# Kernel tuning notes

Hardware: AMD Instinct MI355X
Metric: run time of the kernel (lower is better)

## Reference

```python
import jax, jax.numpy as jnp
import numpy as np

# Config constants from source
L_LAYERS = 4      # n_layer
C = 228           # n_embed
LANES = 4         # SSM.lanes
HD = C // LANES   # head_dim = 57
V = 50257         # vocab_size
B, T = 2, 1024


def _ln(x, g, eps=1e-5):
    # LayerNorm with no bias (bias=False in Block/modules.LayerNorm)
    m = jnp.mean(x, axis=-1, keepdims=True)
    var = jnp.mean((x - m) ** 2, axis=-1, keepdims=True)
    return (x - m) * jax.lax.rsqrt(var + eps) * g


def _rms(z, eps=1e-6):
    # utils.rms: RMS-normalize along last dim
    return z * jax.lax.rsqrt(jnp.mean(z * z, axis=-1, keepdims=True) + eps)


def _combine(left, right, w_orth):
    # SSM.get_scan combine op: per-position lane attention + orthogonal mix + residual
    Bc, Tc, Cc = left.shape
    q = left.reshape(Bc, Tc, LANES, HD)
    k = right.reshape(Bc, Tc, LANES, HD)
    # scanner(left, right, weight): orthogonal butterfly mix of the pair
    v = jnp.einsum('btc,cd->btd', left + right, w_orth).reshape(Bc, Tc, LANES, HD)
    # SDPA over the lane axis (seq length = LANES, feature = HD)
    scores = jnp.einsum('btld,btmd->btlm', q, k) / jnp.sqrt(jnp.float32(HD))
    att = jax.nn.softmax(scores, axis=-1)
    z = jnp.einsum('btlm,btmd->btld', att, v)
    denom = (1.0 + jnp.arange(LANES, dtype=z.dtype)).reshape(1, 1, LANES, 1)
    z = _rms(z) / denom
    return left + z.reshape(Bc, Tc, Cc)


def _pscan2(x, w_orth, ident):
    # log-depth (Kogge-Stone) inclusive scan along time with identity fill
    ident_b = jnp.broadcast_to(ident, x.shape)
    Tn = x.shape[1]
    off = 1
    while off < Tn:  # static python loop: ceil(log2(T)) combine steps
        left = jnp.concatenate([ident_b[:, :off], x[:, :-off]], axis=1)
        x = _combine(left, x, w_orth)
        off *= 2
    return x


def _forward(idx, wte, ln1_g, ln2_g, w_up, w_v, w_cproj, w_scan, ident, w_fc, w_proj):
    x = wte[idx]  # [B,T,C]
    for i in range(L_LAYERS):
        h = _ln(x, ln1_g[i])
        qin = h @ w_up[i].T          # SSM.up
        v = h @ w_v[i].T             # SSM.v_attn
        q = _pscan2(qin, w_scan[i], ident[i])
        y = (q * v) @ w_cproj[i].T   # SSM.c_proj (dropout = identity in eval)
        x = x + y
        h2 = _ln(x, ln2_g[i])
        x = x + jax.nn.gelu(h2 @ w_fc[i].T) @ w_proj[i].T  # MLP
    # lm_head tied to wte (non-Train path applies lm_head directly)
    return x @ wte.T


def setup_inputs() -> dict:
    key = jax.random.key(0)
    ks = jax.random.split(key, 10)
    s = 0.02
    wte = jax.random.normal(ks[0], (V, C), dtype=jnp.float32) * s
    ln1_g = jnp.ones((L_LAYERS, C), dtype=jnp.float32)
    ln2_g = jnp.ones((L_LAYERS, C), dtype=jnp.float32)
    w_up = jax.random.normal(ks[1], (L_LAYERS, C, C), dtype=jnp.float32) * s
    w_v = jax.random.normal(ks[2], (L_LAYERS, C, C), dtype=jnp.float32) * s
    w_cproj = jax.random.normal(ks[3], (L_LAYERS, C, C), dtype=jnp.float32) * s
    # orthogonal scanner weights (compute_orthogonal_weights) via QR
    a = jax.random.normal(ks[4], (L_LAYERS, C, C), dtype=jnp.float32)
    w_scan, _ = jnp.linalg.qr(a)
    ident = jax.random.uniform(ks[5], (L_LAYERS, C), dtype=jnp.float32)  # nn.Parameter(torch.rand)
    w_fc = jax.random.normal(ks[6], (L_LAYERS, 4 * C, C), dtype=jnp.float32) * s
    w_proj = jax.random.normal(ks[7], (L_LAYERS, C, 4 * C), dtype=jnp.float32) * s
    idx = jax.random.randint(ks[8], (B, T), 0, V, dtype=jnp.int64)
    return {"idx": idx, "wte": wte, "ln1_g": ln1_g, "ln2_g": ln2_g, "w_up": w_up,
            "w_v": w_v, "w_cproj": w_cproj, "w_scan": w_scan, "ident": ident,
            "w_fc": w_fc, "w_proj": w_proj}


def reference(idx, wte, ln1_g, ln2_g, w_up, w_v, w_cproj, w_scan, ident, w_fc, w_proj):
    return _forward(idx, wte, ln1_g, ln2_g, w_up, w_v, w_cproj, w_scan, ident, w_fc, w_proj)
```

## Files before the change

### kernel.cpp

```cpp
#include <hip/hip_runtime.h>
#include <hip/hip_bf16.h>

#define C       228
#define TT      1024
#define NPOS    2048
#define LANESN  4
#define HD      57
#define VOC     50257
#define KPAD    256
#define HID     912
#define NLAYER  4

typedef __bf16 bf16x8 __attribute__((ext_vector_type(8)));
typedef float  f32x4  __attribute__((ext_vector_type(4)));

__device__ __forceinline__ float rdl(float v, int lane) {
    return __int_as_float(__builtin_amdgcn_readlane(__float_as_int(v), lane));
}

__global__ void transpose_k(const float* __restrict__ src, float* __restrict__ dst,
                            int R, int Cc, int dstStride, int dstColOff,
                            int srcLayerStride, int dstLayerStride) {
    int layer = blockIdx.y;
    src += (size_t)layer * srcLayerStride;
    dst += (size_t)layer * dstLayerStride;
    int i = blockIdx.x * 256 + threadIdx.x;
    if (i < R * Cc) {
        int r = i / Cc, c = i - r * Cc;
        dst[(size_t)c * dstStride + dstColOff + r] = src[i];
    }
}

__global__ void embed_k(const int* __restrict__ idx, const float* __restrict__ wte,
                        float* __restrict__ x) {
    int i = blockIdx.x * 256 + threadIdx.x;
    int n = i / C, c = i - n * C;
    x[i] = wte[(size_t)idx[n] * C + c];
}

__global__ __launch_bounds__(512) void lnuv_k(const float* __restrict__ x, const float* __restrict__ g,
                                              const float* __restrict__ wuvT,
                                              float* __restrict__ qout, float* __restrict__ vout) {
    __shared__ __align__(16) float hsh[8][256];
    int tid = threadIdx.x, nb = blockIdx.x * 8;
    int wv = tid >> 6, ln = tid & 63;
    const float* xr = x + (size_t)(nb + wv) * C;
    float vals[4]; float s = 0.f, ss = 0.f;
#pragma unroll
    for (int j = 0; j < 4; ++j) {
        int c = ln + 64 * j;
        float vv = (c < C) ? xr[c] : 0.f;
        vals[j] = vv; s += vv; ss += vv * vv;
    }
#pragma unroll
    for (int o = 32; o > 0; o >>= 1) { s += __shfl_xor(s, o, 64); ss += __shfl_xor(ss, o, 64); }
    float mean = s * (1.f / C);
    float rstd = rsqrtf(ss * (1.f / C) - mean * mean + 1e-5f);
#pragma unroll
    for (int j = 0; j < 4; ++j) {
        int c = ln + 64 * j;
        hsh[wv][c] = (c < C) ? (vals[j] - mean) * rstd * g[c] : 0.f;
    }
    __syncthreads();
    f32x4 hv[8];
#pragma unroll
    for (int p = 0; p < 8; ++p) hv[p] = *(const f32x4*)&hsh[p][4 * ln];
    int col  = tid;
    int colc = (col < 2 * C) ? col : 0;
    float acc[8] = {0,0,0,0,0,0,0,0};
    const float* wcol = wuvT + colc;
    for (int c4 = 0; c4 < 57; ++c4) {
        float w0 = wcol[(size_t)(c4 * 4 + 0) * (2 * C)];
        float w1 = wcol[(size_t)(c4 * 4 + 1) * (2 * C)];
        float w2 = wcol[(size_t)(c4 * 4 + 2) * (2 * C)];
        float w3 = wcol[(size_t)(c4 * 4 + 3) * (2 * C)];
#pragma unroll
        for (int p = 0; p < 8; ++p) {
            acc[p] = fmaf(rdl(hv[p].x, c4), w0, acc[p]);
            acc[p] = fmaf(rdl(hv[p].y, c4), w1, acc[p]);
            acc[p] = fmaf(rdl(hv[p].z, c4), w2, acc[p]);
            acc[p] = fmaf(rdl(hv[p].w, c4), w3, acc[p]);
        }
    }
    if (col < C) {
#pragma unroll
        for (int p = 0; p < 8; ++p) qout[(size_t)(nb + p) * C + col] = acc[p];
    } else if (col < 2 * C) {
#pragma unroll
        for (int p = 0; p < 8; ++p) vout[(size_t)(nb + p) * C + col - C] = acc[p];
    }
}

__global__ __launch_bounds__(512) void scan_k(const float* __restrict__ src, float* __restrict__ dst,
                                              const float* __restrict__ wscan,
                                              const float* __restrict__ ident, int off) {
    __shared__ __align__(16) float lsh[8][232];
    __shared__ __align__(16) float rsh[8][232];
    __shared__ __align__(16) float ush[8][256];
    __shared__ __align__(16) float vmsh[8][232];
    __shared__ __align__(16) float zsh[8][232];
    int tid = threadIdx.x;
    int nb  = blockIdx.x * 8;
    int wv = tid >> 6, ln = tid & 63;
    for (int i = tid; i < 8 * C; i += 512) {
        int p = i / C, c = i - p * C;
        int n = nb + p, t = n & (TT - 1);
        float r = src[(size_t)nb * C + i];
        float l = (t >= off) ? src[(size_t)(n - off) * C + c] : ident[c];
        lsh[p][c] = l; rsh[p][c] = r; ush[p][c] = l + r;
    }
    if (tid < 256) { int p = tid >> 5, c = 228 + (tid & 31); if (c < 256) ush[p][c] = 0.f; }
    __syncthreads();
    {
        int half = (tid >= 256) ? 4 : 0;
        int col  = tid & 255;
        int colc = (col < C) ? col : 0;
        f32x4 hv0 = *(const f32x4*)&ush[half + 0][4 * ln];
        f32x4 hv1 = *(const f32x4*)&ush[half + 1][4 * ln];
        f32x4 hv2 = *(const f32x4*)&ush[half + 2][4 * ln];
        f32x4 hv3 = *(const f32x4*)&ush[half + 3][4 * ln];
        float a0 = 0.f, a1 = 0.f, a2 = 0.f, a3 = 0.f;
        const float* wcol = wscan + colc;
        for (int c4 = 0; c4 < 57; ++c4) {
            float w0 = wcol[(size_t)(c4 * 4 + 0) * C];
            float w1 = wcol[(size_t)(c4 * 4 + 1) * C];
            float w2 = wcol[(size_t)(c4 * 4 + 2) * C];
            float w3 = wcol[(size_t)(c4 * 4 + 3) * C];
            a0 = fmaf(rdl(hv0.x, c4), w0, a0); a0 = fmaf(rdl(hv0.y, c4), w1, a0);
            a0 = fmaf(rdl(hv0.z, c4), w2, a0); a0 = fmaf(rdl(hv0.w, c4), w3, a0);
            a1 = fmaf(rdl(hv1.x, c4), w0, a1); a1 = fmaf(rdl(hv1.y, c4), w1, a1);
            a1 = fmaf(rdl(hv1.z, c4), w2, a1); a1 = fmaf(rdl(hv1.w, c4), w3, a1);
            a2 = fmaf(rdl(hv2.x, c4), w0, a2); a2 = fmaf(rdl(hv2.y, c4), w1, a2);
            a2 = fmaf(rdl(hv2.z, c4), w2, a2); a2 = fmaf(rdl(hv2.w, c4), w3, a2);
            a3 = fmaf(rdl(hv3.x, c4), w0, a3); a3 = fmaf(rdl(hv3.y, c4), w1, a3);
            a3 = fmaf(rdl(hv3.z, c4), w2, a3); a3 = fmaf(rdl(hv3.w, c4), w3, a3);
        }
        if (col < C) {
            vmsh[half + 0][col] = a0; vmsh[half + 1][col] = a1;
            vmsh[half + 2][col] = a2; vmsh[half + 3][col] = a3;
        }
    }
    __syncthreads();
    float att = 0.f;
    {
        int l = (ln >> 2) & 3, m = ln & 3;
        float sc = 0.f;
        if (ln < 16) {
            const float* qv = &lsh[wv][l * HD];
            const float* kv = &rsh[wv][m * HD];
            for (int d = 0; d < HD; ++d) sc = fmaf(qv[d], kv[d], sc);
            sc *= 0.13245323570650439f;
        }
        float mx = fmaxf(sc, __shfl_xor(sc, 1, 4));
        mx = fmaxf(mx, __shfl_xor(mx, 2, 4));
        float e = expf(sc - mx);
        float se = e + __shfl_xor(e, 1, 4);
        se += __shfl_xor(se, 2, 4);
        att = e / se;
    }
    float zreg[4];
    int lidx[4];
#pragma unroll
    for (int j = 0; j < 4; ++j) {
        int c = ln + 64 * j;
        zreg[j] = 0.f; lidx[j] = 0;
        if (c < C) {
            int l = (c >= 171) + (c >= 114) + (c >= 57);
            int d = c - 57 * l;
            float b0 = __shfl(att, 4 * l + 0, 64);
            float b1 = __shfl(att, 4 * l + 1, 64);
            float b2 = __shfl(att, 4 * l + 2, 64);
            float b3 = __shfl(att, 4 * l + 3, 64);
            float z = b0 * vmsh[wv][d] + b1 * vmsh[wv][HD + d]
                    + b2 * vmsh[wv][2 * HD + d] + b3 * vmsh[wv][3 * HD + d];
            zsh[wv][c] = z; zreg[j] = z; lidx[j] = l;
        }
    }
    float rs = 0.f;
    if (ln < 4) {
        float zz = 0.f;
        const float* zr = &zsh[wv][ln * HD];
        for (int d = 0; d < HD; ++d) zz = fmaf(zr[d], zr[d], zz);
        rs = rsqrtf(zz * (1.f / HD) + 1e-6f) / (float)(1 + ln);
    }
#pragma unroll
    for (int j = 0; j < 4; ++j) {
        int c = ln + 64 * j;
        if (c < C) {
            float rsl = __shfl(rs, lidx[j], 64);
            dst[(size_t)(nb + wv) * C + c] = lsh[wv][c] + zreg[j] * rsl;
        }
    }
}

__global__ __launch_bounds__(512) void cproj_k(const float* __restrict__ q, const float* __restrict__ v,
                                               const float* __restrict__ wcT, float* __restrict__ x) {
    __shared__ __align__(16) float psh[8][256];
    int tid = threadIdx.x, nb = blockIdx.x * 8;
    int ln = tid & 63;
    for (int i = tid; i < 8 * 256; i += 512) {
        int p = i >> 8, c = i & 255;
        psh[p][c] = (c < C) ? q[(size_t)(nb + p) * C + c] * v[(size_t)(nb + p) * C + c] : 0.f;
    }
    __syncthreads();
    int half = (tid >= 256) ? 4 : 0;
    int col  = tid & 255;
    int colc = (col < C) ? col : 0;
    f32x4 hv0 = *(const f32x4*)&psh[half + 0][4 * ln];
    f32x4 hv1 = *(const f32x4*)&psh[half + 1][4 * ln];
    f32x4 hv2 = *(const f32x4*)&psh[half + 2][4 * ln];
    f32x4 hv3 = *(const f32x4*)&psh[half + 3][4 * ln];
    float a0 = 0.f, a1 = 0.f, a2 = 0.f, a3 = 0.f;
    const float* wcol = wcT + colc;
    for (int c4 = 0; c4 < 57; ++c4) {
        float w0 = wcol[(size_t)(c4 * 4 + 0) * C];
        float w1 = wcol[(size_t)(c4 * 4 + 1) * C];
        float w2 = wcol[(size_t)(c4 * 4 + 2) * C];
        float w3 = wcol[(size_t)(c4 * 4 + 3) * C];
        a0 = fmaf(rdl(hv0.x, c4), w0, a0); a0 = fmaf(rdl(hv0.y, c4), w1, a0);
        a0 = fmaf(rdl(hv0.z, c4), w2, a0); a0 = fmaf(rdl(hv0.w, c4), w3, a0);
        a1 = fmaf(rdl(hv1.x, c4), w0, a1); a1 = fmaf(rdl(hv1.y, c4), w1, a1);
        a1 = fmaf(rdl(hv1.z, c4), w2, a1); a1 = fmaf(rdl(hv1.w, c4), w3, a1);
        a2 = fmaf(rdl(hv2.x, c4), w0, a2); a2 = fmaf(rdl(hv2.y, c4), w1, a2);
        a2 = fmaf(rdl(hv2.z, c4), w2, a2); a2 = fmaf(rdl(hv2.w, c4), w3, a2);
        a3 = fmaf(rdl(hv3.x, c4), w0, a3); a3 = fmaf(rdl(hv3.y, c4), w1, a3);
        a3 = fmaf(rdl(hv3.z, c4), w2, a3); a3 = fmaf(rdl(hv3.w, c4), w3, a3);
    }
    if (col < C) {
        x[(size_t)(nb + half + 0) * C + col] += a0;
        x[(size_t)(nb + half + 1) * C + col] += a1;
        x[(size_t)(nb + half + 2) * C + col] += a2;
        x[(size_t)(nb + half + 3) * C + col] += a3;
    }
}

__global__ __launch_bounds__(512) void lnfc_k(const float* __restrict__ x, const float* __restrict__ g,
                                              const float* __restrict__ wfcT, float* __restrict__ hid) {
    __shared__ __align__(16) float hsh[8][256];
    int tid = threadIdx.x, nb = blockIdx.x * 8;
    int wv = tid >> 6, ln = tid & 63;
    const float* xr = x + (size_t)(nb + wv) * C;
    float vals[4]; float s = 0.f, ss = 0.f;
#pragma unroll
    for (int j = 0; j < 4; ++j) {
        int c = ln + 64 * j;
        float vv = (c < C) ? xr[c] : 0.f;
        vals[j] = vv; s += vv; ss += vv * vv;
    }
#pragma unroll
    for (int o = 32; o > 0; o >>= 1) { s += __shfl_xor(s, o, 64); ss += __shfl_xor(ss, o, 64); }
    float mean = s * (1.f / C);
    float rstd = rsqrtf(ss * (1.f / C) - mean * mean + 1e-5f);
#pragma unroll
    for (int j = 0; j < 4; ++j) {
        int c = ln + 64 * j;
        hsh[wv][c] = (c < C) ? (vals[j] - mean) * rstd * g[c] : 0.f;
    }
    __syncthreads();
    f32x4 hv[8];
#pragma unroll
    for (int p = 0; p < 8; ++p) hv[p] = *(const f32x4*)&hsh[p][4 * ln];
    int c0 = tid;
    int c1 = tid + 512;
    int c1c = (c1 < HID) ? c1 : 0;
    float acc0[8] = {0,0,0,0,0,0,0,0};
    float acc1[8] = {0,0,0,0,0,0,0,0};
    const float* w0p = wfcT + c0;
    const float* w1p = wfcT + c1c;
    for (int c4 = 0; c4 < 57; ++c4) {
        float wa0 = w0p[(size_t)(c4 * 4 + 0) * HID];
        float wa1 = w0p[(size_t)(c4 * 4 + 1) * HID];
        float wa2 = w0p[(size_t)(c4 * 4 + 2) * HID];
        float wa3 = w0p[(size_t)(c4 * 4 + 3) * HID];
        float wb0 = w1p[(size_t)(c4 * 4 + 0) * HID];
        float wb1 = w1p[(size_t)(c4 * 4 + 1) * HID];
        float wb2 = w1p[(size_t)(c4 * 4 + 2) * HID];
        float wb3 = w1p[(size_t)(c4 * 4 + 3) * HID];
#pragma unroll
        for (int p = 0; p < 8; ++p) {
            float h0 = rdl(hv[p].x, c4), h1 = rdl(hv[p].y, c4);
            float h2 = rdl(hv[p].z, c4), h3 = rdl(hv[p].w, c4);
            acc0[p] = fmaf(h0, wa0, acc0[p]); acc0[p] = fmaf(h1, wa1, acc0[p]);
            acc0[p] = fmaf(h2, wa2, acc0[p]); acc0[p] = fmaf(h3, wa3, acc0[p]);
            acc1[p] = fmaf(h0, wb0, acc1[p]); acc1[p] = fmaf(h1, wb1, acc1[p]);
            acc1[p] = fmaf(h2, wb2, acc1[p]); acc1[p] = fmaf(h3, wb3, acc1[p]);
        }
    }
#pragma unroll
    for (int p = 0; p < 8; ++p) {
        float u = acc0[p];
        float th = tanhf(0.7978845608028654f * (u + 0.044715f * u * u * u));
        hid[(size_t)(nb + p) * HID + c0] = 0.5f * u * (1.f + th);
    }
    if (c1 < HID) {
#pragma unroll
        for (int p = 0; p < 8; ++p) {
            float u = acc1[p];
            float th = tanhf(0.7978845608028654f * (u + 0.044715f * u * u * u));
            hid[(size_t)(nb + p) * HID + c1] = 0.5f * u * (1.f + th);
        }
    }
}

__global__ __launch_bounds__(512) void proj_k(const float* __restrict__ hid,
                                              const float* __restrict__ wpT, float* __restrict__ x) {
    __shared__ __align__(16) float hsh[8][944];
    int tid = threadIdx.x, nb = blockIdx.x * 8;
    int ln = tid & 63;
    for (int i = tid; i < 8 * HID; i += 512) {
        int p = i / HID, c = i - p * HID;
        hsh[p][c] = hid[(size_t)nb * HID + i];
    }
    if (tid < 256) { int p = tid >> 5; hsh[p][912 + (tid & 31)] = 0.f; }
    __syncthreads();
    int half = (tid >= 256) ? 4 : 0;
    int col  = tid & 255;
    int colc = (col < C) ? col : 0;
    float a0 = 0.f, a1 = 0.f, a2 = 0.f, a3 = 0.f;
    const float* wcol = wpT + colc;
    for (int ch = 0; ch < 4; ++ch) {
        f32x4 hv0 = *(const f32x4*)&hsh[half + 0][228 * ch + 4 * ln];
        f32x4 hv1 = *(const f32x4*)&hsh[half + 1][228 * ch + 4 * ln];
        f32x4 hv2 = *(const f32x4*)&hsh[half + 2][228 * ch + 4 * ln];
        f32x4 hv3 = *(const f32x4*)&hsh[half + 3][228 * ch + 4 * ln];
        const float* wch = wcol + (size_t)(228 * ch) * C;
        for (int c4 = 0; c4 < 57; ++c4) {
            float w0 = wch[(size_t)(c4 * 4 + 0) * C];
            float w1 = wch[(size_t)(c4 * 4 + 1) * C];
            float w2 = wch[(size_t)(c4 * 4 + 2) * C];
            float w3 = wch[(size_t)(c4 * 4 + 3) * C];
            a0 = fmaf(rdl(hv0.x, c4), w0, a0); a0 = fmaf(rdl(hv0.y, c4), w1, a0);
            a0 = fmaf(rdl(hv0.z, c4), w2, a0); a0 = fmaf(rdl(hv0.w, c4), w3, a0);
            a1 = fmaf(rdl(hv1.x, c4), w0, a1); a1 = fmaf(rdl(hv1.y, c4), w1, a1);
            a1 = fmaf(rdl(hv1.z, c4), w2, a1); a1 = fmaf(rdl(hv1.w, c4), w3, a1);
            a2 = fmaf(rdl(hv2.x, c4), w0, a2); a2 = fmaf(rdl(hv2.y, c4), w1, a2);
            a2 = fmaf(rdl(hv2.z, c4), w2, a2); a2 = fmaf(rdl(hv2.w, c4), w3, a2);
            a3 = fmaf(rdl(hv3.x, c4), w0, a3); a3 = fmaf(rdl(hv3.y, c4), w1, a3);
            a3 = fmaf(rdl(hv3.z, c4), w2, a3); a3 = fmaf(rdl(hv3.w, c4), w3, a3);
        }
    }
    if (col < C) {
        x[(size_t)(nb + half + 0) * C + col] += a0;
        x[(size_t)(nb + half + 1) * C + col] += a1;
        x[(size_t)(nb + half + 2) * C + col] += a2;
        x[(size_t)(nb + half + 3) * C + col] += a3;
    }
}

__global__ void convx_k(const float* __restrict__ x, __hip_bfloat16* __restrict__ xbf) {
    int i = blockIdx.x * 256 + threadIdx.x;
    int n = i >> 8, c = i & 255;
    xbf[i] = __float2bfloat16((c < C) ? x[(size_t)n * C + c] : 0.f);
}
__global__ void convw_k(const float* __restrict__ wte, __hip_bfloat16* __restrict__ wbf) {
    size_t i = (size_t)blockIdx.x * 256 + threadIdx.x;
    size_t n = i >> 8; int c = (int)(i & 255);
    wbf[i] = __float2bfloat16((c < C) ? wte[n * C + c] : 0.f);
}

__global__ __launch_bounds__(256) void lmhead_k(const __bf16* __restrict__ A,
                                                const __bf16* __restrict__ Bw,
                                                float* __restrict__ out) {
    int lane = threadIdx.x & 63;
    int wave = threadIdx.x >> 6;
    int wm = wave >> 1, wn = wave & 1;
    int m0 = blockIdx.x * 128 + wm * 64;
    int n0 = blockIdx.y * 128 + wn * 64;
    int r  = lane & 15, q = lane >> 4;
    f32x4 acc[4][4] = {};
    const __bf16* Ap = A + (size_t)(m0 + r) * KPAD + q * 8;
    int brow[4];
#pragma unroll
    for (int nt = 0; nt < 4; ++nt) { int rw = n0 + nt * 16 + r; brow[nt] = (rw < VOC) ? rw : 0; }
    for (int kc = 0; kc < 8; ++kc) {
        int ko = kc * 32;
        bf16x8 a[4], b[4];
#pragma unroll
        for (int mt = 0; mt < 4; ++mt)
            a[mt] = *(const bf16x8*)(Ap + (size_t)mt * 16 * KPAD + ko);
#pragma unroll
        for (int nt = 0; nt < 4; ++nt)
            b[nt] = *(const bf16x8*)(Bw + (size_t)brow[nt] * KPAD + q * 8 + ko);
#pragma unroll
        for (int mt = 0; mt < 4; ++mt)
#pragma unroll
            for (int nt = 0; nt < 4; ++nt)
                acc[mt][nt] = __builtin_amdgcn_mfma_f32_16x16x32_bf16(a[mt], b[nt], acc[mt][nt], 0, 0, 0);
    }
#pragma unroll
    for (int mt = 0; mt < 4; ++mt)
#pragma unroll
        for (int nt = 0; nt < 4; ++nt) {
            int col = n0 + nt * 16 + r;
            if (col < VOC) {
#pragma unroll
                for (int rr = 0; rr < 4; ++rr) {
                    int row = m0 + mt * 16 + q * 4 + rr;
                    out[(size_t)row * VOC + col] = acc[mt][nt][rr];
                }
            }
        }
}

extern "C" void kernel_launch(void* const* d_in, const int* in_sizes, int n_in,
                              void* d_out, int out_size, void* d_ws, size_t ws_size,
                              hipStream_t stream) {
    const int*   idx     = (const int*)d_in[0];
    const float* wte     = (const float*)d_in[1];
    const float* ln1_g   = (const float*)d_in[2];
    const float* ln2_g   = (const float*)d_in[3];
    const float* w_up    = (const float*)d_in[4];
    const float* w_v     = (const float*)d_in[5];
    const float* w_cproj = (const float*)d_in[6];
    const float* w_scan  = (const float*)d_in[7];
    const float* identp  = (const float*)d_in[8];
    const float* w_fc    = (const float*)d_in[9];
    const float* w_proj  = (const float*)d_in[10];
    float* out = (float*)d_out;

    float* ws   = (float*)d_ws;
    float* x    = ws;
    float* buf0 = x    + (size_t)NPOS * C;
    float* buf1 = buf0 + (size_t)NPOS * C;
    float* vbuf = buf1 + (size_t)NPOS * C;
    float* hid  = vbuf + (size_t)NPOS * C;
    float* wuvT = hid  + (size_t)NPOS * HID;
    float* wcT  = wuvT + (size_t)NLAYER * C * 2 * C;
    float* wfcT = wcT  + (size_t)NLAYER * C * C;
    float* wpT  = wfcT + (size_t)NLAYER * C * HID;
    __hip_bfloat16* xbf   = (__hip_bfloat16*)(wpT + (size_t)NLAYER * HID * C);
    __hip_bfloat16* wtebf = xbf + (size_t)NPOS * KPAD;

    dim3 tg1((C * C + 255) / 256, NLAYER);
    transpose_k<<<tg1, 256, 0, stream>>>(w_up,    wuvT, C, C, 2 * C, 0, C * C, C * 2 * C);
    transpose_k<<<tg1, 256, 0, stream>>>(w_v,     wuvT, C, C, 2 * C, C, C * C, C * 2 * C);
    transpose_k<<<tg1, 256, 0, stream>>>(w_cproj, wcT,  C, C, C,     0, C * C, C * C);
    dim3 tg2((HID * C + 255) / 256, NLAYER);
    transpose_k<<<tg2, 256, 0, stream>>>(w_fc,   wfcT, HID, C, HID, 0, HID * C, C * HID);
    transpose_k<<<tg2, 256, 0, stream>>>(w_proj, wpT,  C, HID, C,   0, C * HID, HID * C);

    embed_k<<<NPOS * C / 256, 256, 0, stream>>>(idx, wte, x);

    for (int L = 0; L < NLAYER; ++L) {
        lnuv_k<<<NPOS / 8, 512, 0, stream>>>(x, ln1_g + L * C, wuvT + (size_t)L * C * 2 * C, buf0, vbuf);
        float* cur = buf0; float* oth = buf1;
        for (int off = 1; off < TT; off <<= 1) {
            scan_k<<<NPOS / 8, 512, 0, stream>>>(cur, oth, w_scan + (size_t)L * C * C, identp + L * C, off);
            float* tmp = cur; cur = oth; oth = tmp;
        }
        cproj_k<<<NPOS / 8, 512, 0, stream>>>(cur, vbuf, wcT + (size_t)L * C * C, x);
        lnfc_k<<<NPOS / 8, 512, 0, stream>>>(x, ln2_g + L * C, wfcT + (size_t)L * C * HID, hid);
        proj_k<<<NPOS / 8, 512, 0, stream>>>(hid, wpT + (size_t)L * HID * C, x);
    }

    convx_k<<<NPOS * KPAD / 256, 256, 0, stream>>>(x, xbf);
    convw_k<<<VOC, 256, 0, stream>>>(wte, wtebf);
    lmhead_k<<<dim3(16, 393), 256, 0, stream>>>((const __bf16*)xbf, (const __bf16*)wtebf, out);
}
```

Before: 1.755 ms.

## Fuse scan steps into cooperative kernel and merge cproj/MLP/next-layer LN-proj

Replaces the ten per-step scan launches per layer with one cooperative kernel that uses grid-wide syncs between steps, falling back to per-step launches if a cooperative launch is unavailable. Merges cproj, LN2+fc+gelu, proj and the next layer's LN1+up/v projection into a single per-row kernel, so the hidden activations stay in shared memory instead of going through a global buffer. Block size drops from 8 rows/512 threads to 4 rows/256 threads. The trade-offs are grid.sync overhead, the occupancy limits that cooperative launch imposes, and a much longer, register-heavy fused kernel.

```diff
diff --git a/kernel.cpp b/kernel.cpp
--- a/kernel.cpp
+++ b/kernel.cpp
@@ -1,5 +1,8 @@
 #include <hip/hip_runtime.h>
 #include <hip/hip_bf16.h>
+#include <hip/hip_cooperative_groups.h>
+
+namespace cg = cooperative_groups;
 
 #define C       228
 #define TT      1024
@@ -10,6 +13,7 @@
 #define KPAD    256
 #define HID     912
 #define NLAYER  4
+#define SCANBLK 512
 
 typedef __bf16 bf16x8 __attribute__((ext_vector_type(8)));
 typedef float  f32x4  __attribute__((ext_vector_type(4)));
@@ -38,11 +42,11 @@
     x[i] = wte[(size_t)idx[n] * C + c];
 }
 
-__global__ __launch_bounds__(512) void lnuv_k(const float* __restrict__ x, const float* __restrict__ g,
+__global__ __launch_bounds__(256) void lnuv_k(const float* __restrict__ x, const float* __restrict__ g,
                                               const float* __restrict__ wuvT,
                                               float* __restrict__ qout, float* __restrict__ vout) {
-    __shared__ __align__(16) float hsh[8][256];
-    int tid = threadIdx.x, nb = blockIdx.x * 8;
+    __shared__ __align__(16) float hsh[4][256];
+    int tid = threadIdx.x, nb = blockIdx.x * 4;
     int wv = tid >> 6, ln = tid & 63;
     const float* xr = x + (size_t)(nb + wv) * C;
     float vals[4]; float s = 0.f, ss = 0.f;
@@ -62,70 +66,66 @@
         hsh[wv][c] = (c < C) ? (vals[j] - mean) * rstd * g[c] : 0.f;
     }
     __syncthreads();
-    f32x4 hv[8];
-#pragma unroll
-    for (int p = 0; p < 8; ++p) hv[p] = *(const f32x4*)&hsh[p][4 * ln];
-    int col  = tid;
-    int colc = (col < 2 * C) ? col : 0;
-    float acc[8] = {0,0,0,0,0,0,0,0};
-    const float* wcol = wuvT + colc;
+    f32x4 hv[4];
+#pragma unroll
+    for (int p = 0; p < 4; ++p) hv[p] = *(const f32x4*)&hsh[p][4 * ln];
+    int col0 = tid, col1 = tid + 256;
+    int c1v = (col1 < 2 * C);
+    float acc0[4] = {0,0,0,0}, acc1[4] = {0,0,0,0};
+    const float* w0p = wuvT + col0;
+    const float* w1p = wuvT + (c1v ? col1 : 0);
     for (int c4 = 0; c4 < 57; ++c4) {
-        float w0 = wcol[(size_t)(c4 * 4 + 0) * (2 * C)];
-        float w1 = wcol[(size_t)(c4 * 4 + 1) * (2 * C)];
-        float w2 = wcol[(size_t)(c4 * 4 + 2) * (2 * C)];
-        float w3 = wcol[(size_t)(c4 * 4 + 3) * (2 * C)];
-#pragma unroll
-        for (int p = 0; p < 8; ++p) {
-            acc[p] = fmaf(rdl(hv[p].x, c4), w0, acc[p]);
-            acc[p] = fmaf(rdl(hv[p].y, c4), w1, acc[p]);
-            acc[p] = fmaf(rdl(hv[p].z, c4), w2, acc[p]);
-            acc[p] = fmaf(rdl(hv[p].w, c4), w3, acc[p]);
-        }
-    }
-    if (col < C) {
-#pragma unroll
-        for (int p = 0; p < 8; ++p) qout[(size_t)(nb + p) * C + col] = acc[p];
-    } else if (col < 2 * C) {
-#pragma unroll
-        for (int p = 0; p < 8; ++p) vout[(size_t)(nb + p) * C + col - C] = acc[p];
-    }
-}
-
-__global__ __launch_bounds__(512) void scan_k(const float* __restrict__ src, float* __restrict__ dst,
-                                              const float* __restrict__ wscan,
-                                              const float* __restrict__ ident, int off) {
-    __shared__ __align__(16) float lsh[8][232];
-    __shared__ __align__(16) float rsh[8][232];
-    __shared__ __align__(16) float ush[8][256];
-    __shared__ __align__(16) float vmsh[8][232];
-    __shared__ __align__(16) float zsh[8][232];
-    int tid = threadIdx.x;
-    int nb  = blockIdx.x * 8;
-    int wv = tid >> 6, ln = tid & 63;
-    for (int i = tid; i < 8 * C; i += 512) {
+        float wa0 = w0p[(size_t)(c4*4+0)*(2*C)], wa1 = w0p[(size_t)(c4*4+1)*(2*C)];
+        float wa2 = w0p[(size_t)(c4*4+2)*(2*C)], wa3 = w0p[(size_t)(c4*4+3)*(2*C)];
+        float wb0 = w1p[(size_t)(c4*4+0)*(2*C)], wb1 = w1p[(size_t)(c4*4+1)*(2*C)];
+        float wb2 = w1p[(size_t)(c4*4+2)*(2*C)], wb3 = w1p[(size_t)(c4*4+3)*(2*C)];
+#pragma unroll
+        for (int p = 0; p < 4; ++p) {
+            float h0 = rdl(hv[p].x, c4), h1 = rdl(hv[p].y, c4);
+            float h2 = rdl(hv[p].z, c4), h3 = rdl(hv[p].w, c4);
+            acc0[p] = fmaf(h0, wa0, acc0[p]); acc0[p] = fmaf(h1, wa1, acc0[p]);
+            acc0[p] = fmaf(h2, wa2, acc0[p]); acc0[p] = fmaf(h3, wa3, acc0[p]);
+            acc1[p] = fmaf(h0, wb0, acc1[p]); acc1[p] = fmaf(h1, wb1, acc1[p]);
+            acc1[p] = fmaf(h2, wb2, acc1[p]); acc1[p] = fmaf(h3, wb3, acc1[p]);
+        }
+    }
+#pragma unroll
+    for (int p = 0; p < 4; ++p) {
+        if (col0 < C) qout[(size_t)(nb+p)*C + col0] = acc0[p];
+        else          vout[(size_t)(nb+p)*C + col0 - C] = acc0[p];
+        if (c1v)      vout[(size_t)(nb+p)*C + col1 - C] = acc1[p];
+    }
+}
+
+__device__ __forceinline__ void scan_step_body(const float* __restrict__ src, float* __restrict__ dst,
+                                               const float* __restrict__ wscan,
+                                               const float* __restrict__ ident, int off,
+                                               int nb, int tid, int wv, int ln,
+                                               float lsh[4][232], float rsh[4][232],
+                                               float ush[4][256], float vmsh[4][232],
+                                               float zsh[4][232]) {
+    for (int i = tid; i < 4 * C; i += 256) {
         int p = i / C, c = i - p * C;
         int n = nb + p, t = n & (TT - 1);
-        float r = src[(size_t)nb * C + i];
+        float r = src[(size_t)n * C + c];
         float l = (t >= off) ? src[(size_t)(n - off) * C + c] : ident[c];
         lsh[p][c] = l; rsh[p][c] = r; ush[p][c] = l + r;
     }
-    if (tid < 256) { int p = tid >> 5, c = 228 + (tid & 31); if (c < 256) ush[p][c] = 0.f; }
-    __syncthreads();
-    {
-        int half = (tid >= 256) ? 4 : 0;
-        int col  = tid & 255;
-        int colc = (col < C) ? col : 0;
-        f32x4 hv0 = *(const f32x4*)&ush[half + 0][4 * ln];
-        f32x4 hv1 = *(const f32x4*)&ush[half + 1][4 * ln];
-        f32x4 hv2 = *(const f32x4*)&ush[half + 2][4 * ln];
-        f32x4 hv3 = *(const f32x4*)&ush[half + 3][4 * ln];
+    if (tid < 128) { int p = tid >> 5, c = 228 + (tid & 31); if (c < 256) ush[p][c] = 0.f; }
+    __syncthreads();
+    {
+        int col = tid, colc = (col < C) ? col : 0;
+        f32x4 hv0 = *(const f32x4*)&ush[0][4 * ln];
+        f32x4 hv1 = *(const f32x4*)&ush[1][4 * ln];
+        f32x4 hv2 = *(const f32x4*)&ush[2][4 * ln];
+        f32x4 hv3 = *(const f32x4*)&ush[3][4 * ln];
         float a0 = 0.f, a1 = 0.f, a2 = 0.f, a3 = 0.f;
         const float* wcol = wscan + colc;
         for (int c4 = 0; c4 < 57; ++c4) {
-            float w0 = wcol[(size_t)(c4 * 4 + 0) * C];
-            float w1 = wcol[(size_t)(c4 * 4 + 1) * C];
-            float w2 = wcol[(size_t)(c4 * 4 + 2) * C];
-            float w3 = wcol[(size_t)(c4 * 4 + 3) * C];
+            float w0 = wcol[(size_t)(c4*4+0)*C];
+            float w1 = wcol[(size_t)(c4*4+1)*C];
+            float w2 = wcol[(size_t)(c4*4+2)*C];
+            float w3 = wcol[(size_t)(c4*4+3)*C];
             a0 = fmaf(rdl(hv0.x, c4), w0, a0); a0 = fmaf(rdl(hv0.y, c4), w1, a0);
             a0 = fmaf(rdl(hv0.z, c4), w2, a0); a0 = fmaf(rdl(hv0.w, c4), w3, a0);
             a1 = fmaf(rdl(hv1.x, c4), w0, a1); a1 = fmaf(rdl(hv1.y, c4), w1, a1);
@@ -135,10 +135,7 @@
             a3 = fmaf(rdl(hv3.x, c4), w0, a3); a3 = fmaf(rdl(hv3.y, c4), w1, a3);
             a3 = fmaf(rdl(hv3.z, c4), w2, a3); a3 = fmaf(rdl(hv3.w, c4), w3, a3);
         }
-        if (col < C) {
-            vmsh[half + 0][col] = a0; vmsh[half + 1][col] = a1;
-            vmsh[half + 2][col] = a2; vmsh[half + 3][col] = a3;
-        }
+        if (col < C) { vmsh[0][col] = a0; vmsh[1][col] = a1; vmsh[2][col] = a2; vmsh[3][col] = a3; }
     }
     __syncthreads();
     float att = 0.f;
@@ -158,8 +155,7 @@
         se += __shfl_xor(se, 2, 4);
         att = e / se;
     }
-    float zreg[4];
-    int lidx[4];
+    float zreg[4]; int lidx[4];
 #pragma unroll
     for (int j = 0; j < 4; ++j) {
         int c = ln + 64 * j;
@@ -193,142 +189,70 @@
     }
 }
 
-__global__ __launch_bounds__(512) void cproj_k(const float* __restrict__ q, const float* __restrict__ v,
-                                               const float* __restrict__ wcT, float* __restrict__ x) {
-    __shared__ __align__(16) float psh[8][256];
-    int tid = threadIdx.x, nb = blockIdx.x * 8;
-    int ln = tid & 63;
-    for (int i = tid; i < 8 * 256; i += 512) {
+__global__ __launch_bounds__(256, 2) void scanfused_k(float* buf0, float* buf1,
+                                                      const float* __restrict__ wscan,
+                                                      const float* __restrict__ ident) {
+    __shared__ __align__(16) float lsh[4][232];
+    __shared__ __align__(16) float rsh[4][232];
+    __shared__ __align__(16) float ush[4][256];
+    __shared__ __align__(16) float vmsh[4][232];
+    __shared__ __align__(16) float zsh[4][232];
+    cg::grid_group grid = cg::this_grid();
+    int tid = threadIdx.x, nb = blockIdx.x * 4;
+    int wv = tid >> 6, ln = tid & 63;
+    const float* src = buf0;
+    float* dst = buf1;
+    for (int off = 1; off < TT; off <<= 1) {
+        scan_step_body(src, dst, wscan, ident, off, nb, tid, wv, ln, lsh, rsh, ush, vmsh, zsh);
+        { const float* t = src; src = dst; dst = (float*)t; }
+        if (off < 512) { grid.sync(); __syncthreads(); }
+    }
+}
+
+__global__ __launch_bounds__(256, 2) void scanstep_k(const float* __restrict__ src, float* __restrict__ dst,
+                                                     const float* __restrict__ wscan,
+                                                     const float* __restrict__ ident, int off) {
+    __shared__ __align__(16) float lsh[4][232];
+    __shared__ __align__(16) float rsh[4][232];
+    __shared__ __align__(16) float ush[4][256];
+    __shared__ __align__(16) float vmsh[4][232];
+    __shared__ __align__(16) float zsh[4][232];
+    int tid = threadIdx.x, nb = blockIdx.x * 4;
+    int wv = tid >> 6, ln = tid & 63;
+    scan_step_body(src, dst, wscan, ident, off, nb, tid, wv, ln, lsh, rsh, ush, vmsh, zsh);
+}
+
+__global__ __launch_bounds__(256) void mlp_k(const float* __restrict__ q, const float* __restrict__ v,
+                                             const float* __restrict__ wcT, const float* __restrict__ g2,
+                                             const float* __restrict__ wfcT, const float* __restrict__ wpT,
+                                             float* __restrict__ x,
+                                             const float* __restrict__ g1n, const float* __restrict__ wuvTn,
+                                             float* __restrict__ qout, float* __restrict__ vout) {
+    __shared__ __align__(16) float psh[4][256];
+    __shared__ __align__(16) float xm[4][232];
+    __shared__ __align__(16) float hsh[4][256];
+    __shared__ __align__(16) float hid[4][944];
+    int tid = threadIdx.x, nb = blockIdx.x * 4;
+    int wv = tid >> 6, ln = tid & 63;
+    for (int i = tid; i < 4 * 256; i += 256) {
         int p = i >> 8, c = i & 255;
         psh[p][c] = (c < C) ? q[(size_t)(nb + p) * C + c] * v[(size_t)(nb + p) * C + c] : 0.f;
     }
-    __syncthreads();
-    int half = (tid >= 256) ? 4 : 0;
-    int col  = tid & 255;
-    int colc = (col < C) ? col : 0;
-    f32x4 hv0 = *(const f32x4*)&psh[half + 0][4 * ln];
-    f32x4 hv1 = *(const f32x4*)&psh[half + 1][4 * ln];
-    f32x4 hv2 = *(const f32x4*)&psh[half + 2][4 * ln];
-    f32x4 hv3 = *(const f32x4*)&psh[half + 3][4 * ln];
-    float a0 = 0.f, a1 = 0.f, a2 = 0.f, a3 = 0.f;
-    const float* wcol = wcT + colc;
-    for (int c4 = 0; c4 < 57; ++c4) {
-        float w0 = wcol[(size_t)(c4 * 4 + 0) * C];
-        float w1 = wcol[(size_t)(c4 * 4 + 1) * C];
-        float w2 = wcol[(size_t)(c4 * 4 + 2) * C];
-        float w3 = wcol[(size_t)(c4 * 4 + 3) * C];
-        a0 = fmaf(rdl(hv0.x, c4), w0, a0); a0 = fmaf(rdl(hv0.y, c4), w1, a0);
-        a0 = fmaf(rdl(hv0.z, c4), w2, a0); a0 = fmaf(rdl(hv0.w, c4), w3, a0);
-        a1 = fmaf(rdl(hv1.x, c4), w0, a1); a1 = fmaf(rdl(hv1.y, c4), w1, a1);
-        a1 = fmaf(rdl(hv1.z, c4), w2, a1); a1 = fmaf(rdl(hv1.w, c4), w3, a1);
-        a2 = fmaf(rdl(hv2.x, c4), w0, a2); a2 = fmaf(rdl(hv2.y, c4), w1, a2);
-        a2 = fmaf(rdl(hv2.z, c4), w2, a2); a2 = fmaf(rdl(hv2.w, c4), w3, a2);
-        a3 = fmaf(rdl(hv3.x, c4), w0, a3); a3 = fmaf(rdl(hv3.y, c4), w1, a3);
-        a3 = fmaf(rdl(hv3.z, c4), w2, a3); a3 = fmaf(rdl(hv3.w, c4), w3, a3);
-    }
-    if (col < C) {
-        x[(size_t)(nb + half + 0) * C + col] += a0;
-        x[(size_t)(nb + half + 1) * C + col] += a1;
-        x[(size_t)(nb + half + 2) * C + col] += a2;
-        x[(size_t)(nb + half + 3) * C + col] += a3;
-    }
-}
-
-__global__ __launch_bounds__(512) void lnfc_k(const float* __restrict__ x, const float* __restrict__ g,
-                                              const float* __restrict__ wfcT, float* __restrict__ hid) {
-    __shared__ __align__(16) float hsh[8][256];
-    int tid = threadIdx.x, nb = blockIdx.x * 8;
-    int wv = tid >> 6, ln = tid & 63;
-    const float* xr = x + (size_t)(nb + wv) * C;
-    float vals[4]; float s = 0.f, ss = 0.f;
-#pragma unroll
-    for (int j = 0; j < 4; ++j) {
-        int c = ln + 64 * j;
-        float vv = (c < C) ? xr[c] : 0.f;
-        vals[j] = vv; s += vv; ss += vv * vv;
-    }
-#pragma unroll
-    for (int o = 32; o > 0; o >>= 1) { s += __shfl_xor(s, o, 64); ss += __shfl_xor(ss, o, 64); }
-    float mean = s * (1.f / C);
-    float rstd = rsqrtf(ss * (1.f / C) - mean * mean + 1e-5f);
-#pragma unroll
-    for (int j = 0; j < 4; ++j) {
-        int c = ln + 64 * j;
-        hsh[wv][c] = (c < C) ? (vals[j] - mean) * rstd * g[c] : 0.f;
-    }
-    __syncthreads();
-    f32x4 hv[8];
-#pragma unroll
-    for (int p = 0; p < 8; ++p) hv[p] = *(const f32x4*)&hsh[p][4 * ln];
-    int c0 = tid;
-    int c1 = tid + 512;
-    int c1c = (c1 < HID) ? c1 : 0;
-    float acc0[8] = {0,0,0,0,0,0,0,0};
-    float acc1[8] = {0,0,0,0,0,0,0,0};
-    const float* w0p = wfcT + c0;
-    const float* w1p = wfcT + c1c;
-    for (int c4 = 0; c4 < 57; ++c4) {
-        float wa0 = w0p[(size_t)(c4 * 4 + 0) * HID];
-        float wa1 = w0p[(size_t)(c4 * 4 + 1) * HID];
-        float wa2 = w0p[(size_t)(c4 * 4 + 2) * HID];
-        float wa3 = w0p[(size_t)(c4 * 4 + 3) * HID];
-        float wb0 = w1p[(size_t)(c4 * 4 + 0) * HID];
-        float wb1 = w1p[(size_t)(c4 * 4 + 1) * HID];
-        float wb2 = w1p[(size_t)(c4 * 4 + 2) * HID];
-        float wb3 = w1p[(size_t)(c4 * 4 + 3) * HID];
-#pragma unroll
-        for (int p = 0; p < 8; ++p) {
-            float h0 = rdl(hv[p].x, c4), h1 = rdl(hv[p].y, c4);
-            float h2 = rdl(hv[p].z, c4), h3 = rdl(hv[p].w, c4);
-            acc0[p] = fmaf(h0, wa0, acc0[p]); acc0[p] = fmaf(h1, wa1, acc0[p]);
-            acc0[p] = fmaf(h2, wa2, acc0[p]); acc0[p] = fmaf(h3, wa3, acc0[p]);
-            acc1[p] = fmaf(h0, wb0, acc1[p]); acc1[p] = fmaf(h1, wb1, acc1[p]);
-            acc1[p] = fmaf(h2, wb2, acc1[p]); acc1[p] = fmaf(h3, wb3, acc1[p]);
-        }
-    }
-#pragma unroll
-    for (int p = 0; p < 8; ++p) {
-        float u = acc0[p];
-        float th = tanhf(0.7978845608028654f * (u + 0.044715f * u * u * u));
-        hid[(size_t)(nb + p) * HID + c0] = 0.5f * u * (1.f + th);
-    }
-    if (c1 < HID) {
-#pragma unroll
-        for (int p = 0; p < 8; ++p) {
-            float u = acc1[p];
-            float th = tanhf(0.7978845608028654f * (u + 0.044715f * u * u * u));
-            hid[(size_t)(nb + p) * HID + c1] = 0.5f * u * (1.f + th);
-        }
-    }
-}
-
-__global__ __launch_bounds__(512) void proj_k(const float* __restrict__ hid,
-                                              const float* __restrict__ wpT, float* __restrict__ x) {
-    __shared__ __align__(16) float hsh[8][944];
-    int tid = threadIdx.x, nb = blockIdx.x * 8;
-    int ln = tid & 63;
-    for (int i = tid; i < 8 * HID; i += 512) {
-        int p = i / HID, c = i - p * HID;
-        hsh[p][c] = hid[(size_t)nb * HID + i];
-    }
-    if (tid < 256) { int p = tid >> 5; hsh[p][912 + (tid & 31)] = 0.f; }
-    __syncthreads();
-    int half = (tid >= 256) ? 4 : 0;
-    int col  = tid & 255;
-    int colc = (col < C) ? col : 0;
-    float a0 = 0.f, a1 = 0.f, a2 = 0.f, a3 = 0.f;
-    const float* wcol = wpT + colc;
-    for (int ch = 0; ch < 4; ++ch) {
-        f32x4 hv0 = *(const f32x4*)&hsh[half + 0][228 * ch + 4 * ln];
-        f32x4 hv1 = *(const f32x4*)&hsh[half + 1][228 * ch + 4 * ln];
-        f32x4 hv2 = *(const f32x4*)&hsh[half + 2][228 * ch + 4 * ln];
-        f32x4 hv3 = *(const f32x4*)&hsh[half + 3][228 * ch + 4 * ln];
-        const float* wch = wcol + (size_t)(228 * ch) * C;
+    if (tid < 128) { int p = tid >> 5; hid[p][912 + (tid & 31)] = 0.f; }
+    __syncthreads();
+    {
+        int col = tid, colc = (col < C) ? col : 0;
+        f32x4 hv0 = *(const f32x4*)&psh[0][4 * ln];
+        f32x4 hv1 = *(const f32x4*)&psh[1][4 * ln];
+        f32x4 hv2 = *(const f32x4*)&psh[2][4 * ln];
+        f32x4 hv3 = *(const f32x4*)&psh[3][4 * ln];
+        float a0 = 0.f, a1 = 0.f, a2 = 0.f, a3 = 0.f;
+        const float* wcol = wcT + colc;
         for (int c4 = 0; c4 < 57; ++c4) {
-            float w0 = wch[(size_t)(c4 * 4 + 0) * C];
-            float w1 = wch[(size_t)(c4 * 4 + 1) * C];
-            float w2 = wch[(size_t)(c4 * 4 + 2) * C];
-            float w3 = wch[(size_t)(c4 * 4 + 3) * C];
+            float w0 = wcol[(size_t)(c4*4+0)*C];
+            float w1 = wcol[(size_t)(c4*4+1)*C];
+            float w2 = wcol[(size_t)(c4*4+2)*C];
+            float w3 = wcol[(size_t)(c4*4+3)*C];
             a0 = fmaf(rdl(hv0.x, c4), w0, a0); a0 = fmaf(rdl(hv0.y, c4), w1, a0);
             a0 = fmaf(rdl(hv0.z, c4), w2, a0); a0 = fmaf(rdl(hv0.w, c4), w3, a0);
             a1 = fmaf(rdl(hv1.x, c4), w0, a1); a1 = fmaf(rdl(hv1.y, c4), w1, a1);
@@ -338,12 +262,159 @@
             a3 = fmaf(rdl(hv3.x, c4), w0, a3); a3 = fmaf(rdl(hv3.y, c4), w1, a3);
             a3 = fmaf(rdl(hv3.z, c4), w2, a3); a3 = fmaf(rdl(hv3.w, c4), w3, a3);
         }
-    }
-    if (col < C) {
-        x[(size_t)(nb + half + 0) * C + col] += a0;
-        x[(size_t)(nb + half + 1) * C + col] += a1;
-        x[(size_t)(nb + half + 2) * C + col] += a2;
-        x[(size_t)(nb + half + 3) * C + col] += a3;
+        if (col < C) {
+            xm[0][col] = x[(size_t)(nb+0)*C + col] + a0;
+            xm[1][col] = x[(size_t)(nb+1)*C + col] + a1;
+            xm[2][col] = x[(size_t)(nb+2)*C + col] + a2;
+            xm[3][col] = x[(size_t)(nb+3)*C + col] + a3;
+        }
+    }
+    __syncthreads();
+    {
+        float vals[4]; float s = 0.f, ss = 0.f;
+#pragma unroll
+        for (int j = 0; j < 4; ++j) {
+            int c = ln + 64 * j;
+            float vv = (c < C) ? xm[wv][c] : 0.f;
+            vals[j] = vv; s += vv; ss += vv * vv;
+        }
+#pragma unroll
+        for (int o = 32; o > 0; o >>= 1) { s += __shfl_xor(s, o, 64); ss += __shfl_xor(ss, o, 64); }
+        float mean = s * (1.f / C);
+        float rstd = rsqrtf(ss * (1.f / C) - mean * mean + 1e-5f);
+#pragma unroll
+        for (int j = 0; j < 4; ++j) {
+            int c = ln + 64 * j;
+            hsh[wv][c] = (c < C) ? (vals[j] - mean) * rstd * g2[c] : 0.f;
+        }
+    }
+    __syncthreads();
+    {
+        f32x4 hv[4];
+#pragma unroll
+        for (int p = 0; p < 4; ++p) hv[p] = *(const f32x4*)&hsh[p][4 * ln];
+        int c0 = tid, c1 = tid + 256, c2 = tid + 512, c3 = tid + 768;
+        int c3v = (c3 < HID);
+        const float* wp0 = wfcT + c0;
+        const float* wp1 = wfcT + c1;
+        const float* wp2 = wfcT + c2;
+        const float* wp3 = wfcT + (c3v ? c3 : 0);
+        float acc[4][4] = {};
+        for (int c4 = 0; c4 < 57; ++c4) {
+            float wa0 = wp0[(size_t)(c4*4+0)*HID], wa1 = wp0[(size_t)(c4*4+1)*HID];
+            float wa2 = wp0[(size_t)(c4*4+2)*HID], wa3 = wp0[(size_t)(c4*4+3)*HID];
+            float wb0 = wp1[(size_t)(c4*4+0)*HID], wb1 = wp1[(size_t)(c4*4+1)*HID];
+            float wb2 = wp1[(size_t)(c4*4+2)*HID], wb3 = wp1[(size_t)(c4*4+3)*HID];
+            float wc0 = wp2[(size_t)(c4*4+0)*HID], wc1 = wp2[(size_t)(c4*4+1)*HID];
+            float wc2 = wp2[(size_t)(c4*4+2)*HID], wc3 = wp2[(size_t)(c4*4+3)*HID];
+            float wd0 = wp3[(size_t)(c4*4+0)*HID], wd1 = wp3[(size_t)(c4*4+1)*HID];
+            float wd2 = wp3[(size_t)(c4*4+2)*HID], wd3 = wp3[(size_t)(c4*4+3)*HID];
+#pragma unroll
+            for (int p = 0; p < 4; ++p) {
+                float h0 = rdl(hv[p].x, c4), h1 = rdl(hv[p].y, c4);
+                float h2 = rdl(hv[p].z, c4), h3 = rdl(hv[p].w, c4);
+                acc[0][p] = fmaf(h0, wa0, acc[0][p]); acc[0][p] = fmaf(h1, wa1, acc[0][p]);
+                acc[0][p] = fmaf(h2, wa2, acc[0][p]); acc[0][p] = fmaf(h3, wa3, acc[0][p]);
+                acc[1][p] = fmaf(h0, wb0, acc[1][p]); acc[1][p] = fmaf(h1, wb1, acc[1][p]);
+                acc[1][p] = fmaf(h2, wb2, acc[1][p]); acc[1][p] = fmaf(h3, wb3, acc[1][p]);
+                acc[2][p] = fmaf(h0, wc0, acc[2][p]); acc[2][p] = fmaf(h1, wc1, acc[2][p]);
+                acc[2][p] = fmaf(h2, wc2, acc[2][p]); acc[2][p] = fmaf(h3, wc3, acc[2][p]);
+                acc[3][p] = fmaf(h0, wd0, acc[3][p]); acc[3][p] = fmaf(h1, wd1, acc[3][p]);
+                acc[3][p] = fmaf(h2, wd2, acc[3][p]); acc[3][p] = fmaf(h3, wd3, acc[3][p]);
+            }
+        }
+#pragma unroll
+        for (int p = 0; p < 4; ++p) {
+            float u0 = acc[0][p], u1 = acc[1][p], u2 = acc[2][p], u3 = acc[3][p];
+            hid[p][c0] = 0.5f * u0 * (1.f + tanhf(0.7978845608028654f * (u0 + 0.044715f * u0 * u0 * u0)));
+            hid[p][c1] = 0.5f * u1 * (1.f + tanhf(0.7978845608028654f * (u1 + 0.044715f * u1 * u1 * u1)));
+            hid[p][c2] = 0.5f * u2 * (1.f + tanhf(0.7978845608028654f * (u2 + 0.044715f * u2 * u2 * u2)));
+            if (c3v) hid[p][c3] = 0.5f * u3 * (1.f + tanhf(0.7978845608028654f * (u3 + 0.044715f * u3 * u3 * u3)));
+        }
+    }
+    __syncthreads();
+    {
+        int col = tid, colc = (col < C) ? col : 0;
+        float a[4] = {0,0,0,0};
+        const float* wcol = wpT + colc;
+        for (int ch = 0; ch < 4; ++ch) {
+            f32x4 hv[4];
+#pragma unroll
+            for (int p = 0; p < 4; ++p) hv[p] = *(const f32x4*)&hid[p][228 * ch + 4 * ln];
+            const float* wch = wcol + (size_t)(228 * ch) * C;
+            for (int c4 = 0; c4 < 57; ++c4) {
+                float w0 = wch[(size_t)(c4*4+0)*C];
+                float w1 = wch[(size_t)(c4*4+1)*C];
+                float w2 = wch[(size_t)(c4*4+2)*C];
+                float w3 = wch[(size_t)(c4*4+3)*C];
+#pragma unroll
+                for (int p = 0; p < 4; ++p) {
+                    a[p] = fmaf(rdl(hv[p].x, c4), w0, a[p]);
+                    a[p] = fmaf(rdl(hv[p].y, c4), w1, a[p]);
+                    a[p] = fmaf(rdl(hv[p].z, c4), w2, a[p]);
+                    a[p] = fmaf(rdl(hv[p].w, c4), w3, a[p]);
+                }
+            }
+        }
+        if (col < C) {
+#pragma unroll
+            for (int p = 0; p < 4; ++p) {
+                float xf = xm[p][col] + a[p];
+                x[(size_t)(nb + p) * C + col] = xf;
+                psh[p][col] = xf;
+            }
+        }
+    }
+    if (qout != nullptr) {
+        __syncthreads();
+        {
+            float vals[4]; float s = 0.f, ss = 0.f;
+#pragma unroll
+            for (int j = 0; j < 4; ++j) {
+                int c = ln + 64 * j;
+                float vv = (c < C) ? psh[wv][c] : 0.f;
+                vals[j] = vv; s += vv; ss += vv * vv;
+            }
+#pragma unroll
+            for (int o = 32; o > 0; o >>= 1) { s += __shfl_xor(s, o, 64); ss += __shfl_xor(ss, o, 64); }
+            float mean = s * (1.f / C);
+            float rstd = rsqrtf(ss * (1.f / C) - mean * mean + 1e-5f);
+#pragma unroll
+            for (int j = 0; j < 4; ++j) {
+                int c = ln + 64 * j;
+                hsh[wv][c] = (c < C) ? (vals[j] - mean) * rstd * g1n[c] : 0.f;
+            }
+        }
+        __syncthreads();
+        f32x4 hv[4];
+#pragma unroll
+        for (int p = 0; p < 4; ++p) hv[p] = *(const f32x4*)&hsh[p][4 * ln];
+        int col0 = tid, col1 = tid + 256;
+        int c1v = (col1 < 2 * C);
+        float acc0[4] = {0,0,0,0}, acc1[4] = {0,0,0,0};
+        const float* w0p = wuvTn + col0;
+        const float* w1p = wuvTn + (c1v ? col1 : 0);
+        for (int c4 = 0; c4 < 57; ++c4) {
+            float wa0 = w0p[(size_t)(c4*4+0)*(2*C)], wa1 = w0p[(size_t)(c4*4+1)*(2*C)];
+            float wa2 = w0p[(size_t)(c4*4+2)*(2*C)], wa3 = w0p[(size_t)(c4*4+3)*(2*C)];
+            float wb0 = w1p[(size_t)(c4*4+0)*(2*C)], wb1 = w1p[(size_t)(c4*4+1)*(2*C)];
+            float wb2 = w1p[(size_t)(c4*4+2)*(2*C)], wb3 = w1p[(size_t)(c4*4+3)*(2*C)];
+#pragma unroll
+            for (int p = 0; p < 4; ++p) {
+                float h0 = rdl(hv[p].x, c4), h1 = rdl(hv[p].y, c4);
+                float h2 = rdl(hv[p].z, c4), h3 = rdl(hv[p].w, c4);
+                acc0[p] = fmaf(h0, wa0, acc0[p]); acc0[p] = fmaf(h1, wa1, acc0[p]);
+                acc0[p] = fmaf(h2, wa2, acc0[p]); acc0[p] = fmaf(h3, wa3, acc0[p]);
+                acc1[p] = fmaf(h0, wb0, acc1[p]); acc1[p] = fmaf(h1, wb1, acc1[p]);
+                acc1[p] = fmaf(h2, wb2, acc1[p]); acc1[p] = fmaf(h3, wb3, acc1[p]);
+            }
+        }
+#pragma unroll
+        for (int p = 0; p < 4; ++p) {
+            if (col0 < C) qout[(size_t)(nb+p)*C + col0] = acc0[p];
+            else          vout[(size_t)(nb+p)*C + col0 - C] = acc0[p];
+            if (c1v)      vout[(size_t)(nb+p)*C + col1 - C] = acc1[p];
+        }
     }
 }
 
@@ -423,13 +494,19 @@
     float* buf0 = x    + (size_t)NPOS * C;
     float* buf1 = buf0 + (size_t)NPOS * C;
     float* vbuf = buf1 + (size_t)NPOS * C;
-    float* hid  = vbuf + (size_t)NPOS * C;
-    float* wuvT = hid  + (size_t)NPOS * HID;
+    float* wuvT = vbuf + (size_t)NPOS * C;
     float* wcT  = wuvT + (size_t)NLAYER * C * 2 * C;
     float* wfcT = wcT  + (size_t)NLAYER * C * C;
     float* wpT  = wfcT + (size_t)NLAYER * C * HID;
     __hip_bfloat16* xbf   = (__hip_bfloat16*)(wpT + (size_t)NLAYER * HID * C);
     __hip_bfloat16* wtebf = xbf + (size_t)NPOS * KPAD;
+
+    int coop = 0;
+    {
+        int dev = 0;
+        hipGetDevice(&dev);
+        hipDeviceGetAttribute(&coop, hipDeviceAttributeCooperativeLaunch, dev);
+    }
 
     dim3 tg1((C * C + 255) / 256, NLAYER);
     transpose_k<<<tg1, 256, 0, stream>>>(w_up,    wuvT, C, C, 2 * C, 0, C * C, C * 2 * C);
@@ -441,16 +518,36 @@
 
     embed_k<<<NPOS * C / 256, 256, 0, stream>>>(idx, wte, x);
 
+    lnuv_k<<<NPOS / 4, 256, 0, stream>>>(x, ln1_g, wuvT, buf0, vbuf);
     for (int L = 0; L < NLAYER; ++L) {
-        lnuv_k<<<NPOS / 8, 512, 0, stream>>>(x, ln1_g + L * C, wuvT + (size_t)L * C * 2 * C, buf0, vbuf);
-        float* cur = buf0; float* oth = buf1;
-        for (int off = 1; off < TT; off <<= 1) {
-            scan_k<<<NPOS / 8, 512, 0, stream>>>(cur, oth, w_scan + (size_t)L * C * C, identp + L * C, off);
-            float* tmp = cur; cur = oth; oth = tmp;
-        }
-        cproj_k<<<NPOS / 8, 512, 0, stream>>>(cur, vbuf, wcT + (size_t)L * C * C, x);
-        lnfc_k<<<NPOS / 8, 512, 0, stream>>>(x, ln2_g + L * C, wfcT + (size_t)L * C * HID, hid);
-        proj_k<<<NPOS / 8, 512, 0, stream>>>(hid, wpT + (size_t)L * HID * C, x);
+        const float* wscan_l = w_scan + (size_t)L * C * C;
+        const float* ident_l = identp + (size_t)L * C;
+        bool fused_ok = false;
+        if (coop) {
+            float* a0 = buf0; float* a1 = buf1;
+            void* args[] = { &a0, &a1, (void*)&wscan_l, (void*)&ident_l };
+            hipError_t e = hipLaunchCooperativeKernel((const void*)scanfused_k,
+                                                      dim3(SCANBLK), dim3(256), args, 0, stream);
+            fused_ok = (e == hipSuccess);
+        }
+        if (!fused_ok) {
+            float* cur = buf0; float* oth = buf1;
+            for (int off = 1; off < TT; off <<= 1) {
+                scanstep_k<<<NPOS / 4, 256, 0, stream>>>(cur, oth, wscan_l, ident_l, off);
+                float* t = cur; cur = oth; oth = t;
+            }
+        }
+        bool last = (L == NLAYER - 1);
+        mlp_k<<<NPOS / 4, 256, 0, stream>>>(buf0, vbuf,
+                                            wcT  + (size_t)L * C * C,
+                                            ln2_g + L * C,
+                                            wfcT + (size_t)L * C * HID,
+                                            wpT  + (size_t)L * HID * C,
+                                            x,
+                                            last ? nullptr : (ln1_g + (size_t)(L + 1) * C),
+                                            last ? nullptr : (wuvT + (size_t)(L + 1) * C * 2 * C),
+                                            last ? nullptr : buf0,
+                                            last ? nullptr : vbuf);
     }
 
     convx_k<<<NPOS * KPAD / 256, 256, 0, stream>>>(x, xbf);
```

Result: slower. 3.756 ms (+114.1%).
